# Kernel tuning notes

Measured on AMD Instinct MI355X. Metric: run time of the kernel, lower is better.

Reference implementation:

```python
import jax, jax.numpy as jnp
import numpy as np

IDIM = 1024
HIDDEN = 4096
N_EXPERT = 8
T = 2048


def setup_inputs() -> dict:
    key = jax.random.key(0)
    ks = jax.random.split(key, 6)
    s_in = 1.0 / np.sqrt(IDIM)
    s_h = 1.0 / np.sqrt(HIDDEN)
    return {
        "xs": jax.random.normal(ks[0], (T, IDIM), dtype=jnp.float32),
        "top_k": 2,
        # gate: Linear(idim -> n_expert, bias=False); torch weight (E, D)
        "Wg": jax.random.uniform(ks[1], (N_EXPERT, IDIM), jnp.float32, -s_in, s_in),
        # experts stacked: w_1 Linear(idim->hidden), w_2 Linear(hidden->idim)
        "W1": jax.random.uniform(ks[2], (N_EXPERT, IDIM, HIDDEN), jnp.float32, -s_in, s_in),
        "b1": jax.random.uniform(ks[3], (N_EXPERT, HIDDEN), jnp.float32, -s_in, s_in),
        "W2": jax.random.uniform(ks[4], (N_EXPERT, HIDDEN, IDIM), jnp.float32, -s_h, s_h),
        "b2": jax.random.uniform(ks[5], (N_EXPERT, IDIM), jnp.float32, -s_h, s_h),
    }


def reference(xs, top_k, Wg, W1, b1, W2, b2):
    # Router: (T, E)
    router = xs @ Wg.T
    logits, selected = jax.lax.top_k(router, top_k)          # (T, k)
    # softmax over the top-k slot axis in fp32, cast back (matches torch)
    weights = jax.nn.softmax(logits.astype(jnp.float32), axis=-1).astype(xs.dtype)
    # combine weight per token per expert: (T, E). Tokens not routed to an
    # expert get weight 0, zeroing that expert's contribution (same math as
    # the masked gather / scatter-add in the torch loop).
    onehot = jax.nn.one_hot(selected, N_EXPERT, dtype=xs.dtype)  # (T, k, E)
    comb = jnp.einsum("tk,tke->te", weights, onehot)
    # all-expert FFN (dropout_rate = 0 -> identity)
    h = jax.nn.relu(jnp.einsum("td,edh->teh", xs, W1) + b1[None, :, :])
    y = jnp.einsum("teh,ehd->ted", h, W2) + b2[None, :, :]
    return jnp.einsum("te,ted->td", comb, y)
```

## Files before the change

### kernel.cpp

```cpp
#include <hip/hip_runtime.h>
#include <stdint.h>

#define T_TOK 2048
#define IDIM  1024
#define HID   4096
#define NE    8
#define BM    128
#define BN    128
#define BN2   64
#define BK    64
#define RMAX  5120
#define MAXTILES 40

typedef __bf16 bf16;
typedef bf16  bf16x8 __attribute__((ext_vector_type(8)));
typedef float f32x4  __attribute__((ext_vector_type(4)));

#define WS_NTILES   128
#define WS_TILE_E   192
#define WS_TILE_R   448
#define WS_TOK_E    1024
#define WS_TOK_W    17408
#define WS_ROW_TOK  33792
#define WS_ROW_W    54272
#define WS_TOK_POS  74752
#define XG_OFF      131072

__device__ __forceinline__ int xcd_remap(int orig, int nwg) {
    int q = nwg >> 3, r = nwg & 7;
    int xcd = orig & 7, idx = orig >> 3;
    return (xcd < r ? xcd * (q + 1) : r * (q + 1) + (xcd - r) * q) + idx;
}

__global__ __launch_bounds__(256) void k_router(const float* __restrict__ xs,
                                                const float* __restrict__ Wg,
                                                int* __restrict__ tok_e,
                                                float* __restrict__ tok_w) {
    __shared__ float sWg[NE * IDIM];
    for (int i = threadIdx.x; i < NE * IDIM; i += 256) sWg[i] = Wg[i];
    __syncthreads();
    int wave = threadIdx.x >> 6, lane = threadIdx.x & 63;
    int t = blockIdx.x * 4 + wave;
    if (t >= T_TOK) return;
    float p[NE];
#pragma unroll
    for (int e = 0; e < NE; e++) p[e] = 0.f;
    for (int j = 0; j < IDIM / 64; j++) {
        float x = xs[(size_t)t * IDIM + j * 64 + lane];
#pragma unroll
        for (int e = 0; e < NE; e++)
            p[e] += x * sWg[e * IDIM + j * 64 + lane];
    }
#pragma unroll
    for (int e = 0; e < NE; e++) {
        float v = p[e];
        for (int off = 32; off > 0; off >>= 1) v += __shfl_down(v, off);
        p[e] = v;
    }
    if (lane == 0) {
        int e0 = 0; float l0 = p[0];
        for (int e = 1; e < NE; e++) if (p[e] > l0) { l0 = p[e]; e0 = e; }
        int e1 = -1; float l1 = -1e30f;
        for (int e = 0; e < NE; e++) if (e != e0 && p[e] > l1) { l1 = p[e]; e1 = e; }
        if (e1 < 0) e1 = (e0 + 1) & 7;
        float z = __expf(l1 - l0);
        tok_e[2 * t]     = e0;  tok_e[2 * t + 1] = e1;
        tok_w[2 * t]     = 1.f / (1.f + z);
        tok_w[2 * t + 1] = z / (1.f + z);
    }
}

__global__ __launch_bounds__(256) void k_setup(int* __restrict__ w,
                                               float* __restrict__ wf) {
    __shared__ int cnt[NE];
    __shared__ int cur[NE];
    int tid = threadIdx.x;
    if (tid < NE) cnt[tid] = 0;
    for (int i = tid; i < RMAX; i += 256) w[WS_ROW_TOK / 4 + i] = -1;
    __syncthreads();
    for (int i = tid; i < 2 * T_TOK; i += 256)
        atomicAdd(&cnt[w[WS_TOK_E / 4 + i]], 1);
    __syncthreads();
    if (tid == 0) {
        int off = 0, nt = 0;
        for (int e = 0; e < NE; e++) {
            cur[e] = off;
            int nb = (cnt[e] + BM - 1) / BM;
            for (int b = 0; b < nb && nt < MAXTILES; b++) {
                w[WS_TILE_E / 4 + nt] = e;
                w[WS_TILE_R / 4 + nt] = off + b * BM;
                nt++;
            }
            off += nb * BM;
        }
        w[WS_NTILES / 4] = nt;
    }
    __syncthreads();
    for (int i = tid; i < 2 * T_TOK; i += 256) {
        int e   = w[WS_TOK_E / 4 + i];
        int pos = atomicAdd(&cur[e], 1);
        if (pos < RMAX) {
            w[WS_ROW_TOK / 4 + pos] = i >> 1;
            wf[WS_ROW_W / 4 + pos]  = wf[WS_TOK_W / 4 + i];
            w[WS_TOK_POS / 4 + i]   = pos;
        } else {
            w[WS_TOK_POS / 4 + i]   = 0;
        }
    }
}

__device__ inline uint4 pack8(float4 a, float4 b) {
    union { bf16 h[8]; uint4 u; } pk;
    pk.h[0] = (bf16)a.x; pk.h[1] = (bf16)a.y; pk.h[2] = (bf16)a.z; pk.h[3] = (bf16)a.w;
    pk.h[4] = (bf16)b.x; pk.h[5] = (bf16)b.y; pk.h[6] = (bf16)b.z; pk.h[7] = (bf16)b.w;
    return pk.u;
}
__device__ inline uint32_t pack2(float a, float b) {
    union { bf16 h[2]; uint32_t u; } pk;
    pk.h[0] = (bf16)a; pk.h[1] = (bf16)b;
    return pk.u;
}

__device__ __forceinline__ void g2l16(const bf16* g, bf16* l) {
    __builtin_amdgcn_global_load_lds(
        (const __attribute__((address_space(1))) void*)g,
        (__attribute__((address_space(3))) void*)l, 16, 0, 0);
}

__global__ __launch_bounds__(256) void k_gather(const float* __restrict__ xs,
                                                const int* __restrict__ wsi,
                                                bf16* __restrict__ Xg) {
    int wv = threadIdx.x >> 6, lane = threadIdx.x & 63;
    int r = blockIdx.x * 4 + wv;
    int tok = wsi[WS_ROW_TOK / 4 + r];
#pragma unroll
    for (int i = 0; i < 2; i++) {
        int c = i * 64 + lane;
        uint4 v;
        if (tok >= 0) {
            const float* g = xs + (size_t)tok * IDIM + c * 8;
            v = pack8(*(const float4*)g, *(const float4*)(g + 4));
        } else v = make_uint4(0u, 0u, 0u, 0u);
        int cs = (c & ~7) | ((c & 7) ^ (r & 7));
        *(uint4*)&Xg[(size_t)r * IDIM + cs * 8] = v;
    }
}

__global__ __launch_bounds__(256) void k_cvt(const float* __restrict__ src,
                                             bf16* __restrict__ dst,
                                             int ld_src, int k0, int n0, int KL,
                                             size_t s_estride, size_t d_estride,
                                             int tpb) {
    __shared__ bf16 sT[64 * 66];
    int e = blockIdx.z;
    const float* S = src + (size_t)e * s_estride;
    bf16* D = dst + (size_t)e * d_estride;
    int tn  = blockIdx.x;
    int tk0 = blockIdx.y * tpb;
    int t = threadIdx.x;
    for (int tt = 0; tt < tpb; tt++) {
        int tk = tk0 + tt;
        if (tt) __syncthreads();
#pragma unroll
        for (int i = 0; i < 4; i++) {
            int idx = t + i * 256;
            int k = idx >> 4, n4 = (idx & 15) * 4;
            float4 v = *(const float4*)&S[(size_t)(k0 + tk * 64 + k) * ld_src +
                                          n0 + tn * 64 + n4];
            *(uint32_t*)&sT[k * 66 + n4]     = pack2(v.x, v.y);
            *(uint32_t*)&sT[k * 66 + n4 + 2] = pack2(v.z, v.w);
        }
        __syncthreads();
#pragma unroll
        for (int j = 0; j < 2; j++) {
            int idx = t + j * 256;
            int n = idx >> 3, kq = idx & 7;
            union { bf16 h[8]; uint4 u; } pk;
#pragma unroll
            for (int jj = 0; jj < 8; jj++) pk.h[jj] = sT[(kq * 8 + jj) * 66 + n];
            int ng = tn * 64 + n;
            int ch = kq ^ (ng & 7);
            *(uint4*)&D[(size_t)ng * KL + tk * 64 + ch * 8] = pk.u;
        }
    }
}

__global__ __launch_bounds__(256) void k_ffn1n(const bf16* __restrict__ Xg,
                                               const bf16* __restrict__ W1t,
                                               const float* __restrict__ b1,
                                               const int* __restrict__ wsi,
                                               bf16* __restrict__ H,
                                               int h0, int CW) {
    int gx = gridDim.x;
    int orig = blockIdx.x + gx * blockIdx.y;
    int wgid = xcd_remap(orig, gx * gridDim.y);
    int bx = wgid % gx, tile = wgid / gx;
    if (tile >= wsi[WS_NTILES / 4]) return;
    int e    = wsi[WS_TILE_E / 4 + tile];
    int row0 = wsi[WS_TILE_R / 4 + tile];
    int n0   = bx * BN;

    const bf16* Abase = Xg + (size_t)row0 * IDIM;
    const bf16* Bbase = W1t + ((size_t)e * CW + n0) * IDIM;

    __shared__ bf16 sA[2][BM * BK];
    __shared__ bf16 sB[2][BN * BK];

    int t = threadIdx.x, lane = t & 63;
    int wv = t >> 6, wx = wv & 1, wy = wv >> 1;
    int lm = lane & 15, q = lane >> 4;

    f32x4 acc[4][4];
#pragma unroll
    for (int i = 0; i < 4; i++)
#pragma unroll
        for (int j = 0; j < 4; j++) acc[i][j] = (f32x4){0.f, 0.f, 0.f, 0.f};

    auto stage = [&](int kc, int b) {
#pragma unroll
        for (int i = 0; i < 4; i++) {
            int s = t + i * 256;
            g2l16(Abase + (size_t)(s >> 3) * IDIM + kc * BK + (s & 7) * 8,
                  &sA[b][s * 8]);
        }
#pragma unroll
        for (int i = 0; i < 4; i++) {
            int s = t + i * 256;
            g2l16(Bbase + (size_t)(s >> 3) * IDIM + kc * BK + (s & 7) * 8,
                  &sB[b][s * 8]);
        }
    };

    stage(0, 0);
    __syncthreads();
    for (int kc = 0; kc < IDIM / BK; kc++) {
        int cur = kc & 1;
        if (kc + 1 < IDIM / BK) stage(kc + 1, cur ^ 1);
        const bf16* A = sA[cur];
        const bf16* B = sB[cur];
#pragma unroll
        for (int ks = 0; ks < 2; ks++) {
            bf16x8 aF[4], bF[4];
#pragma unroll
            for (int mt = 0; mt < 4; mt++) {
                int r = wy * 64 + mt * 16 + lm;
                aF[mt] = *(const bf16x8*)&A[r * BK + (((ks * 4 + q) ^ (r & 7)) * 8)];
            }
#pragma unroll
            for (int nt = 0; nt < 4; nt++) {
                int r = wx * 64 + nt * 16 + lm;
                bF[nt] = *(const bf16x8*)&B[r * BK + (((ks * 4 + q) ^ (r & 7)) * 8)];
            }
#pragma unroll
            for (int mt = 0; mt < 4; mt++)
#pragma unroll
                for (int nt = 0; nt < 4; nt++)
                    acc[mt][nt] = __builtin_amdgcn_mfma_f32_16x16x32_bf16(
                        aF[mt], bF[nt], acc[mt][nt], 0, 0, 0);
        }
        __syncthreads();
    }

    bf16* sC = &sA[0][0];
#pragma unroll
    for (int nt = 0; nt < 4; nt++) {
        int col_l = wx * 64 + nt * 16 + lm;
        float bv  = b1[(size_t)e * HID + h0 + n0 + col_l];
#pragma unroll
        for (int mt = 0; mt < 4; mt++) {
#pragma unroll
            for (int r = 0; r < 4; r++) {
                int rloc = wy * 64 + mt * 16 + q * 4 + r;
                int rg   = row0 + rloc;
                float v = fmaxf(acc[mt][nt][r] + bv, 0.f);
                int sc = (col_l & ~63) | ((col_l & 63) ^ ((rg & 7) << 3));
                sC[rloc * BN + sc] = (bf16)v;
            }
        }
    }
    __syncthreads();
#pragma unroll
    for (int i = 0; i < 8; i++) {
        int u = t + i * 256;
        int row = u >> 4, c = u & 15;
        uint4 v = *(const uint4*)&sC[row * BN + c * 8];
        *(uint4*)&H[(size_t)(row0 + row) * CW + n0 + c * 8] = v;
    }
}

__global__ __launch_bounds__(256) void k_ffn2y(const bf16* __restrict__ H,
                                               const bf16* __restrict__ W2t,
                                               const float* __restrict__ b2,
                                               const int* __restrict__ wsi,
                                               float* __restrict__ Y,
                                               int CW, int first) {
    int gx = gridDim.x;
    int orig = blockIdx.x + gx * blockIdx.y;
    int wgid = xcd_remap(orig, gx * gridDim.y);
    int bx = wgid % gx, tile = wgid / gx;
    if (tile >= wsi[WS_NTILES / 4]) return;
    int e    = wsi[WS_TILE_E / 4 + tile];
    int row0 = wsi[WS_TILE_R / 4 + tile];
    int n0   = bx * BN2;

    const bf16* Abase = H + (size_t)row0 * CW;
    const bf16* Bbase = W2t + ((size_t)e * IDIM + n0) * CW;

    __shared__ bf16 sA[2][BM * BK];
    __shared__ bf16 sB[2][BN2 * BK];

    int t = threadIdx.x, lane = t & 63;
    int wv = t >> 6, wx = wv & 1, wy = wv >> 1;
    int lm = lane & 15, q = lane >> 4;

    f32x4 acc[4][2];
#pragma unroll
    for (int i = 0; i < 4; i++)
#pragma unroll
        for (int j = 0; j < 2; j++) acc[i][j] = (f32x4){0.f, 0.f, 0.f, 0.f};

    auto stage = [&](int kc, int b) {
#pragma unroll
        for (int i = 0; i < 4; i++) {
            int s = t + i * 256;
            g2l16(Abase + (size_t)(s >> 3) * CW + kc * BK + (s & 7) * 8,
                  &sA[b][s * 8]);
        }
#pragma unroll
        for (int i = 0; i < 2; i++) {
            int s = t + i * 256;
            g2l16(Bbase + (size_t)(s >> 3) * CW + kc * BK + (s & 7) * 8,
                  &sB[b][s * 8]);
        }
    };

    int kiters = CW / BK;
    stage(0, 0);
    __syncthreads();
    for (int kc = 0; kc < kiters; kc++) {
        int cur = kc & 1;
        if (kc + 1 < kiters) stage(kc + 1, cur ^ 1);
        const bf16* A = sA[cur];
        const bf16* B = sB[cur];
#pragma unroll
        for (int ks = 0; ks < 2; ks++) {
            bf16x8 aF[4], bF[2];
#pragma unroll
            for (int mt = 0; mt < 4; mt++) {
                int r = wy * 64 + mt * 16 + lm;
                aF[mt] = *(const bf16x8*)&A[r * BK + (((ks * 4 + q) ^ (r & 7)) * 8)];
            }
#pragma unroll
            for (int nt = 0; nt < 2; nt++) {
                int r = wx * 32 + nt * 16 + lm;
                bF[nt] = *(const bf16x8*)&B[r * BK + (((ks * 4 + q) ^ (r & 7)) * 8)];
            }
#pragma unroll
            for (int mt = 0; mt < 4; mt++)
#pragma unroll
                for (int nt = 0; nt < 2; nt++)
                    acc[mt][nt] = __builtin_amdgcn_mfma_f32_16x16x32_bf16(
                        aF[mt], bF[nt], acc[mt][nt], 0, 0, 0);
        }
        __syncthreads();
    }

#pragma unroll
    for (int nt = 0; nt < 2; nt++) {
        int col  = n0 + wx * 32 + nt * 16 + lm;
        float bv = first ? b2[(size_t)e * IDIM + col] : 0.f;
#pragma unroll
        for (int mt = 0; mt < 4; mt++)
#pragma unroll
            for (int r = 0; r < 4; r++) {
                int rg = row0 + wy * 64 + mt * 16 + q * 4 + r;
                float* p = &Y[(size_t)rg * IDIM + col];
                float v  = acc[mt][nt][r] + bv;
                *p = first ? v : (*p + v);
            }
    }
}

__global__ __launch_bounds__(256) void k_combine(const float* __restrict__ Y,
                                                 const int* __restrict__ wsi,
                                                 const float* __restrict__ wsf,
                                                 float* __restrict__ out) {
    int tok = blockIdx.x;
    int p0 = wsi[WS_TOK_POS / 4 + 2 * tok];
    int p1 = wsi[WS_TOK_POS / 4 + 2 * tok + 1];
    float w0 = wsf[WS_TOK_W / 4 + 2 * tok];
    float w1 = wsf[WS_TOK_W / 4 + 2 * tok + 1];
    int c = threadIdx.x;
    const float4* y0 = (const float4*)(Y + (size_t)p0 * IDIM);
    const float4* y1 = (const float4*)(Y + (size_t)p1 * IDIM);
    float4 a = y0[c], b = y1[c];
    float4 r;
    r.x = w0 * a.x + w1 * b.x;
    r.y = w0 * a.y + w1 * b.y;
    r.z = w0 * a.z + w1 * b.z;
    r.w = w0 * a.w + w1 * b.w;
    ((float4*)(out + (size_t)tok * IDIM))[c] = r;
}

__global__ __launch_bounds__(256) void k_fallback(const float* __restrict__ xs,
                                                  const float* __restrict__ Wg,
                                                  const float* __restrict__ W1,
                                                  const float* __restrict__ b1,
                                                  const float* __restrict__ W2,
                                                  const float* __restrict__ b2,
                                                  float* __restrict__ out) {
    __shared__ float xbuf[IDIM];
    __shared__ float hbuf[256];
    __shared__ float slog[NE];
    __shared__ int   sel[2];
    __shared__ float selw[2];

    int t   = blockIdx.x;
    int tid = threadIdx.x;

    for (int i = tid; i < IDIM; i += 256)
        xbuf[i] = xs[(size_t)t * IDIM + i];
    __syncthreads();
    {
        int e = tid >> 5, l = tid & 31;
        float p = 0.f;
        for (int d = l; d < IDIM; d += 32)
            p += xbuf[d] * Wg[e * IDIM + d];
        for (int off = 16; off > 0; off >>= 1) p += __shfl_down(p, off, 32);
        if (l == 0) slog[e] = p;
    }
    __syncthreads();
    if (tid == 0) {
        int e0 = 0; float l0 = slog[0];
        for (int e = 1; e < NE; e++) if (slog[e] > l0) { l0 = slog[e]; e0 = e; }
        int e1 = -1; float l1 = -1e30f;
        for (int e = 0; e < NE; e++) if (e != e0 && slog[e] > l1) { l1 = slog[e]; e1 = e; }
        if (e1 < 0) e1 = (e0 + 1) & 7;
        float z = __expf(l1 - l0);
        sel[0] = e0; sel[1] = e1;
        selw[0] = 1.f / (1.f + z);
        selw[1] = z / (1.f + z);
    }
    __syncthreads();

    float ytot[4] = {0.f, 0.f, 0.f, 0.f};
#pragma unroll
    for (int s = 0; s < 2; s++) {
        int   e = sel[s];
        float w = selw[s];
        const float* W1e = W1 + (size_t)e * IDIM * HID;
        const float* W2e = W2 + (size_t)e * HID * IDIM;
        float ys[4] = {0.f, 0.f, 0.f, 0.f};
        for (int hb = 0; hb < HID / 256; hb++) {
            int h = hb * 256 + tid;
            float acc = b1[e * HID + h];
            for (int d = 0; d < IDIM; d++)
                acc += xbuf[d] * W1e[(size_t)d * HID + h];
            __syncthreads();
            hbuf[tid] = fmaxf(acc, 0.f);
            __syncthreads();
            for (int hh = 0; hh < 256; hh++) {
                float hv = hbuf[hh];
                const float* wrow = W2e + (size_t)(hb * 256 + hh) * IDIM;
#pragma unroll
                for (int cc = 0; cc < 4; cc++)
                    ys[cc] += hv * wrow[cc * 256 + tid];
            }
        }
#pragma unroll
        for (int cc = 0; cc < 4; cc++)
            ytot[cc] += w * (ys[cc] + b2[e * IDIM + cc * 256 + tid]);
    }
#pragma unroll
    for (int cc = 0; cc < 4; cc++)
        out[(size_t)t * IDIM + cc * 256 + tid] = ytot[cc];
}

extern "C" void kernel_launch(void* const* d_in, const int* in_sizes, int n_in,
                              void* d_out, int out_size, void* d_ws, size_t ws_size,
                              hipStream_t stream) {
    int o = (n_in >= 7 && in_sizes[1] == 1) ? 1 : 0;
    const float* xs = (const float*)d_in[0];
    const float* Wg = (const float*)d_in[1 + o];
    const float* W1 = (const float*)d_in[2 + o];
    const float* b1 = (const float*)d_in[3 + o];
    const float* W2 = (const float*)d_in[4 + o];
    const float* b2 = (const float*)d_in[5 + o];
    float* out = (float*)d_out;

    size_t xg_sz = (size_t)RMAX * IDIM * 2;
    size_t y_sz  = (size_t)RMAX * IDIM * 4;
    int CW = 0;
    if (d_ws) {
        for (int c = HID; c >= 512; c >>= 1) {
            size_t need = (size_t)XG_OFF + xg_sz + (size_t)RMAX * c * 2 +
                          (size_t)NE * c * IDIM * 2 + y_sz;
            if (ws_size >= need) { CW = c; break; }
        }
    }
    if (!CW) {
        k_fallback<<<T_TOK, 256, 0, stream>>>(xs, Wg, W1, b1, W2, b2, out);
        return;
    }

    char*  ws  = (char*)d_ws;
    int*   wsi = (int*)d_ws;
    float* wsf = (float*)d_ws;
    bf16*  Xg  = (bf16*)(ws + XG_OFF);
    bf16*  Hb  = (bf16*)(ws + XG_OFF + xg_sz);
    bf16*  Wt  = (bf16*)(ws + XG_OFF + xg_sz + (size_t)RMAX * CW * 2);
    float* Yb  = (float*)(ws + XG_OFF + xg_sz + (size_t)RMAX * CW * 2 +
                          (size_t)NE * CW * IDIM * 2);

    k_router<<<T_TOK / 4, 256, 0, stream>>>(xs, Wg, wsi + WS_TOK_E / 4,
                                            wsf + WS_TOK_W / 4);
    k_setup<<<1, 256, 0, stream>>>(wsi, wsf);
    k_gather<<<RMAX / 4, 256, 0, stream>>>(xs, wsi, Xg);

    int HC = HID / CW;
    for (int c = 0; c < HC; c++) {
        {
            int ntn = CW / 64, ntk = IDIM / 64;
            int tpb = ntk;
            while (ntn * NE * (ntk / tpb) < 1024 && tpb > 1) tpb >>= 1;
            k_cvt<<<dim3(ntn, ntk / tpb, NE), 256, 0, stream>>>(
                W1, Wt, HID, 0, c * CW, IDIM,
                (size_t)IDIM * HID, (size_t)CW * IDIM, tpb);
        }
        k_ffn1n<<<dim3(CW / BN, MAXTILES), 256, 0, stream>>>(
            Xg, Wt, b1, wsi, Hb, c * CW, CW);
        {
            int ntn = IDIM / 64, ntk = CW / 64;
            int tpb = ntk;
            while (ntn * NE * (ntk / tpb) < 1024 && tpb > 1) tpb >>= 1;
            k_cvt<<<dim3(ntn, ntk / tpb, NE), 256, 0, stream>>>(
                W2, Wt, IDIM, c * CW, 0, CW,
                (size_t)HID * IDIM, (size_t)IDIM * CW, tpb);
        }
        k_ffn2y<<<dim3(IDIM / BN2, MAXTILES), 256, 0, stream>>>(
            Hb, Wt, b2, wsi, Yb, CW, c == 0 ? 1 : 0);
    }
    k_combine<<<T_TOK, 256, 0, stream>>>(Yb, wsi, wsf, out);
}
```

Before: 455.8 us.

## Replace double-buffered LDS staging with single buffer in both FFN GEMMs

Removes the double-buffered shared-memory prefetch in both expert GEMM kernels and uses one LDS buffer per operand instead. Each iteration loads its tile, syncs, computes, then syncs before the next load. This halves LDS use per workgroup, which may allow more resident workgroups per CU to hide latency. In exchange, the explicit overlap between the next tile's global loads and the current tile's MFMA work is lost.

```diff
diff --git a/kernel.cpp b/kernel.cpp
--- a/kernel.cpp
+++ b/kernel.cpp
@@ -203,8 +203,9 @@
     const bf16* Abase = Xg + (size_t)row0 * IDIM;
     const bf16* Bbase = W1t + ((size_t)e * CW + n0) * IDIM;
 
-    __shared__ bf16 sA[2][BM * BK];
-    __shared__ bf16 sB[2][BN * BK];
+    __shared__ bf16 smem[BM * BK + BN * BK];
+    bf16* sA = smem;
+    bf16* sB = smem + BM * BK;
 
     int t = threadIdx.x, lane = t & 63;
     int wv = t >> 6, wx = wv & 1, wy = wv >> 1;
@@ -216,40 +217,33 @@
 #pragma unroll
         for (int j = 0; j < 4; j++) acc[i][j] = (f32x4){0.f, 0.f, 0.f, 0.f};
 
-    auto stage = [&](int kc, int b) {
+    for (int kc = 0; kc < IDIM / BK; kc++) {
+        if (kc) __syncthreads();
 #pragma unroll
         for (int i = 0; i < 4; i++) {
             int s = t + i * 256;
             g2l16(Abase + (size_t)(s >> 3) * IDIM + kc * BK + (s & 7) * 8,
-                  &sA[b][s * 8]);
+                  &sA[s * 8]);
         }
 #pragma unroll
         for (int i = 0; i < 4; i++) {
             int s = t + i * 256;
             g2l16(Bbase + (size_t)(s >> 3) * IDIM + kc * BK + (s & 7) * 8,
-                  &sB[b][s * 8]);
-        }
-    };
-
-    stage(0, 0);
-    __syncthreads();
-    for (int kc = 0; kc < IDIM / BK; kc++) {
-        int cur = kc & 1;
-        if (kc + 1 < IDIM / BK) stage(kc + 1, cur ^ 1);
-        const bf16* A = sA[cur];
-        const bf16* B = sB[cur];
+                  &sB[s * 8]);
+        }
+        __syncthreads();
 #pragma unroll
         for (int ks = 0; ks < 2; ks++) {
             bf16x8 aF[4], bF[4];
 #pragma unroll
             for (int mt = 0; mt < 4; mt++) {
                 int r = wy * 64 + mt * 16 + lm;
-                aF[mt] = *(const bf16x8*)&A[r * BK + (((ks * 4 + q) ^ (r & 7)) * 8)];
+                aF[mt] = *(const bf16x8*)&sA[r * BK + (((ks * 4 + q) ^ (r & 7)) * 8)];
             }
 #pragma unroll
             for (int nt = 0; nt < 4; nt++) {
                 int r = wx * 64 + nt * 16 + lm;
-                bF[nt] = *(const bf16x8*)&B[r * BK + (((ks * 4 + q) ^ (r & 7)) * 8)];
+                bF[nt] = *(const bf16x8*)&sB[r * BK + (((ks * 4 + q) ^ (r & 7)) * 8)];
             }
 #pragma unroll
             for (int mt = 0; mt < 4; mt++)
@@ -258,10 +252,10 @@
                     acc[mt][nt] = __builtin_amdgcn_mfma_f32_16x16x32_bf16(
                         aF[mt], bF[nt], acc[mt][nt], 0, 0, 0);
         }
-        __syncthreads();
-    }
-
-    bf16* sC = &sA[0][0];
+    }
+
+    __syncthreads();
+    bf16* sC = smem;
 #pragma unroll
     for (int nt = 0; nt < 4; nt++) {
         int col_l = wx * 64 + nt * 16 + lm;
@@ -306,8 +300,8 @@
     const bf16* Abase = H + (size_t)row0 * CW;
     const bf16* Bbase = W2t + ((size_t)e * IDIM + n0) * CW;
 
-    __shared__ bf16 sA[2][BM * BK];
-    __shared__ bf16 sB[2][BN2 * BK];
+    __shared__ bf16 sA[BM * BK];
+    __shared__ bf16 sB[BN2 * BK];
 
     int t = threadIdx.x, lane = t & 63;
     int wv = t >> 6, wx = wv & 1, wy = wv >> 1;
@@ -319,41 +313,34 @@
 #pragma unroll
         for (int j = 0; j < 2; j++) acc[i][j] = (f32x4){0.f, 0.f, 0.f, 0.f};
 
-    auto stage = [&](int kc, int b) {
+    int kiters = CW / BK;
+    for (int kc = 0; kc < kiters; kc++) {
+        if (kc) __syncthreads();
 #pragma unroll
         for (int i = 0; i < 4; i++) {
             int s = t + i * 256;
             g2l16(Abase + (size_t)(s >> 3) * CW + kc * BK + (s & 7) * 8,
-                  &sA[b][s * 8]);
+                  &sA[s * 8]);
         }
 #pragma unroll
         for (int i = 0; i < 2; i++) {
             int s = t + i * 256;
             g2l16(Bbase + (size_t)(s >> 3) * CW + kc * BK + (s & 7) * 8,
-                  &sB[b][s * 8]);
-        }
-    };
-
-    int kiters = CW / BK;
-    stage(0, 0);
-    __syncthreads();
-    for (int kc = 0; kc < kiters; kc++) {
-        int cur = kc & 1;
-        if (kc + 1 < kiters) stage(kc + 1, cur ^ 1);
-        const bf16* A = sA[cur];
-        const bf16* B = sB[cur];
+                  &sB[s * 8]);
+        }
+        __syncthreads();
 #pragma unroll
         for (int ks = 0; ks < 2; ks++) {
             bf16x8 aF[4], bF[2];
 #pragma unroll
             for (int mt = 0; mt < 4; mt++) {
                 int r = wy * 64 + mt * 16 + lm;
-                aF[mt] = *(const bf16x8*)&A[r * BK + (((ks * 4 + q) ^ (r & 7)) * 8)];
+                aF[mt] = *(const bf16x8*)&sA[r * BK + (((ks * 4 + q) ^ (r & 7)) * 8)];
             }
 #pragma unroll
             for (int nt = 0; nt < 2; nt++) {
                 int r = wx * 32 + nt * 16 + lm;
-                bF[nt] = *(const bf16x8*)&B[r * BK + (((ks * 4 + q) ^ (r & 7)) * 8)];
+                bF[nt] = *(const bf16x8*)&sB[r * BK + (((ks * 4 + q) ^ (r & 7)) * 8)];
             }
 #pragma unroll
             for (int mt = 0; mt < 4; mt++)
@@ -362,7 +349,6 @@
                     acc[mt][nt] = __builtin_amdgcn_mfma_f32_16x16x32_bf16(
                         aF[mt], bF[nt], acc[mt][nt], 0, 0, 0);
         }
-        __syncthreads();
     }
 
 #pragma unroll
```

After: 438.2 us. 3.9% less time.
